# Optimization experiments

Hardware: AMD Instinct MI355X
Metric: run time of the kernel (lower is better)

The kernel has to match this reference:

```python
import jax, jax.numpy as jnp
import numpy as np
from jax import lax

B, T, E, H, L = 32, 512, 1024, 1024, 128


def setup_inputs() -> dict:
    key = jax.random.key(0)
    ks = jax.random.split(key, 25)
    s = 0.02  # small init scale for stable tanh/sigmoid

    def p(k, shape):
        return jax.random.normal(k, shape, jnp.float32) * s

    return {
        "x": jax.random.normal(ks[0], (B, T, E), jnp.float32),
        "eps": jax.random.normal(ks[1], (B, L), jnp.float32),
        # linear1 / linear2 (torch convention: W is [out, in])
        "W1": p(ks[2], (H, E)), "b1": jnp.zeros((H,), jnp.float32),
        "W2": p(ks[3], (H, H)), "b2": jnp.zeros((H,), jnp.float32),
        # encoder GRU (gates ordered r,z,n as in torch)
        "Wih_e": p(ks[4], (3 * H, H)), "Whh_e": p(ks[5], (3 * H, H)),
        "bih_e": jnp.zeros((3 * H,), jnp.float32), "bhh_e": jnp.zeros((3 * H,), jnp.float32),
        # decoder GRU
        "Wih_d": p(ks[6], (3 * H, H)), "Whh_d": p(ks[7], (3 * H, H)),
        "bih_d": jnp.zeros((3 * H,), jnp.float32), "bhh_d": jnp.zeros((3 * H,), jnp.float32),
        # VAE heads
        "Wm": p(ks[8], (L, H)), "bm": jnp.zeros((L,), jnp.float32),
        "Wv": p(ks[9], (L, H)), "bv": jnp.zeros((L,), jnp.float32),
        "Wl": p(ks[10], (H, L)), "bl": jnp.zeros((H,), jnp.float32),
        # output layer (H -> E)
        "Wo": p(ks[11], (E, H)), "bo": jnp.zeros((E,), jnp.float32),
        "lengths": jax.random.randint(ks[12], (B,), 1, T + 1, jnp.int32),
    }


def _gru(xs, h0, Wih, Whh, bih, bhh, lengths):
    """torch-style GRU over padded batch xs:[B,T,H].
    Emulates pack_padded_sequence: h frozen and outputs zeroed for t >= length.
    Returns (outputs [B,T,H], final hidden [B,H])."""
    Tn = xs.shape[1]

    def step(h, inp):
        xt, t = inp  # xt:[B,H]
        gi = xt @ Wih.T + bih          # [B,3H]
        gh = h @ Whh.T + bhh           # [B,3H]
        ir, iz, inn = jnp.split(gi, 3, axis=-1)
        hr, hz, hn = jnp.split(gh, 3, axis=-1)
        r = jax.nn.sigmoid(ir + hr)
        zg = jax.nn.sigmoid(iz + hz)
        n = jnp.tanh(inn + r * hn)
        hnew = (1.0 - zg) * n + zg * h
        valid = (t < lengths)[:, None]
        hout = jnp.where(valid, hnew, h)
        yout = jnp.where(valid, hnew, 0.0)  # pad_packed padding_value=0.0
        return hout, yout

    hT, ys = lax.scan(step, h0, (xs.transpose(1, 0, 2), jnp.arange(Tn)))
    return ys.transpose(1, 0, 2), hT


def reference(x, eps, W1, b1, W2, b2, Wih_e, Whh_e, bih_e, bhh_e,
              Wih_d, Whh_d, bih_d, bhh_d, Wm, bm, Wv, bv, Wl, bl, Wo, bo,
              lengths):
    # pad() sorts the batch by descending length (stable) for packing
    sorted_idx = jnp.argsort(-lengths)
    rev_idx = jnp.argsort(sorted_idx)
    xs = x[sorted_idx]            # sorted padded input
    ls = lengths[sorted_idx]

    # shared input projection linear2(relu(linear1(.)))  (decoder dropout is eval-mode identity)
    proj = jnp.maximum(xs @ W1.T + b1, 0.0) @ W2.T + b2   # [B,T,H]

    h0 = jnp.zeros((xs.shape[0], H), proj.dtype)
    _, h_enc = _gru(proj, h0, Wih_e, Whh_e, bih_e, bhh_e, ls)  # [B,H]

    mean = h_enc @ Wm.T + bm
    logv = h_enc @ Wv.T + bv
    z = eps * jnp.exp(0.5 * logv) + mean                   # [B,L], sorted order
    dec_h0 = z @ Wl.T + bl                                 # [B,H]

    ys, _ = _gru(proj, dec_h0, Wih_d, Whh_d, bih_d, bhh_d, ls)  # [B,T,H]
    outputs_layer = ys[rev_idx] @ Wo.T + bo                # unsorted, [B,T,E]

    return (x, outputs_layer, mean, logv, z)
```

## Files before the change

kernel.cpp:

```cpp
#include <hip/hip_runtime.h>
#include <stdint.h>

#define B_  32
#define T_  512
#define E_  1024
#define H_  1024
#define L_  128
#define BT  (B_*T_)
#define G3  (3*H_)

typedef float f32x4 __attribute__((ext_vector_type(4)));
typedef short bf16x8 __attribute__((ext_vector_type(8)));

__device__ __forceinline__ unsigned short f2bf(float f) {
  unsigned u = __float_as_uint(f);
  u = (u + 0x7fffu + ((u >> 16) & 1u)) >> 16;
  return (unsigned short)u;
}
__device__ __forceinline__ float bf2f(unsigned short s) {
  return __uint_as_float(((unsigned)s) << 16);
}

__global__ void k_f2bf(const float* __restrict__ in, unsigned short* __restrict__ out, int n) {
  int i = (blockIdx.x * blockDim.x + threadIdx.x) * 4;
  if (i >= n) return;
  float4 v = *(const float4*)(in + i);
  unsigned lo = (unsigned)f2bf(v.x) | ((unsigned)f2bf(v.y) << 16);
  unsigned hi = (unsigned)f2bf(v.z) | ((unsigned)f2bf(v.w) << 16);
  *(uint2*)(out + i) = make_uint2(lo, hi);
}

template<int OUT_F32, int RELU>
__global__ __launch_bounds__(256)
void k_gemm(const unsigned short* __restrict__ A, const unsigned short* __restrict__ W,
            const float* __restrict__ bias, void* __restrict__ Cc,
            int M, int N, int K)
{
  __shared__ __align__(16) unsigned short As[128 * 64];
  __shared__ __align__(16) unsigned short Bs[128 * 64];
  const int m0 = blockIdx.x * 128, n0 = blockIdx.y * 128;
  const int tid = threadIdx.x;
  const int lane = tid & 63, wv = tid >> 6;
  const int wr = wv >> 1, wc = wv & 1;
  f32x4 acc[4][4] = {};

  for (int k0 = 0; k0 < K; k0 += 64) {
#pragma unroll
    for (int i = 0; i < 4; ++i) {
      int o = tid * 16 + i * 4096;
      int r = o >> 7;
      int cb = o & 127;
      const unsigned short* ga = A + (size_t)(m0 + r) * K + k0 + (cb >> 1);
      const unsigned short* gb = W + (size_t)(n0 + r) * K + k0 + (cb >> 1);
      __builtin_amdgcn_global_load_lds((const __attribute__((address_space(1))) void*)ga,
          (__attribute__((address_space(3))) void*)((char*)As + o), 16, 0, 0);
      __builtin_amdgcn_global_load_lds((const __attribute__((address_space(1))) void*)gb,
          (__attribute__((address_space(3))) void*)((char*)Bs + o), 16, 0, 0);
    }
    __syncthreads();
#pragma unroll
    for (int kk = 0; kk < 2; ++kk) {
      bf16x8 af[4], bfr[4];
#pragma unroll
      for (int m = 0; m < 4; ++m)
        af[m] = *(const bf16x8*)(As + (wr * 64 + m * 16 + (lane & 15)) * 64 + kk * 32 + (lane >> 4) * 8);
#pragma unroll
      for (int n = 0; n < 4; ++n)
        bfr[n] = *(const bf16x8*)(Bs + (wc * 64 + n * 16 + (lane & 15)) * 64 + kk * 32 + (lane >> 4) * 8);
#pragma unroll
      for (int m = 0; m < 4; ++m)
#pragma unroll
        for (int n = 0; n < 4; ++n)
          acc[m][n] = __builtin_amdgcn_mfma_f32_16x16x32_bf16(af[m], bfr[n], acc[m][n], 0, 0, 0);
    }
    __syncthreads();
  }
#pragma unroll
  for (int m = 0; m < 4; ++m) {
    int row0 = m0 + wr * 64 + m * 16 + (lane >> 4) * 4;
#pragma unroll
    for (int n = 0; n < 4; ++n) {
      int col = n0 + wc * 64 + n * 16 + (lane & 15);
      float bvv = bias[col];
#pragma unroll
      for (int q = 0; q < 4; ++q) {
        float v = acc[m][n][q] + bvv;
        if (RELU) v = fmaxf(v, 0.f);
        size_t idx = (size_t)(row0 + q) * N + col;
        if (OUT_F32) ((float*)Cc)[idx] = v;
        else ((unsigned short*)Cc)[idx] = f2bf(v);
      }
    }
  }
}

__device__ __forceinline__ void gbar(unsigned* bar, unsigned target) {
  __syncthreads();
  if (threadIdx.x == 0) {
    __hip_atomic_fetch_add(bar, 1u, __ATOMIC_ACQ_REL, __HIP_MEMORY_SCOPE_AGENT);
    while (__hip_atomic_load(bar, __ATOMIC_ACQUIRE, __HIP_MEMORY_SCOPE_AGENT) < target) {
      __builtin_amdgcn_s_sleep(8);
    }
  }
  __syncthreads();
}

template<int IS_DEC>
__global__ __launch_bounds__(384, 2)
void k_gru(const unsigned short* __restrict__ gi,
           const unsigned short* __restrict__ Whhb,
           const float* __restrict__ bhh,
           const int* __restrict__ lengths,
           const float* __restrict__ h0,
           float* __restrict__ hT,
           unsigned short* __restrict__ ys,
           unsigned short* __restrict__ hbuf,
           unsigned* __restrict__ bar)
{
  const int wg = blockIdx.x;
  const int U0 = wg * 16;
  const int tid = threadIdx.x;
  const int lane = tid & 63, wv = tid >> 6;
  const int mt = wv & 1, g = wv >> 1;

  __shared__ float gh_lds[32][48];
  __shared__ float h_master[32][16];
  __shared__ float bhh_s[48];
  __shared__ int len_s[32];

  if (tid < 32) len_s[tid] = lengths[tid];
  if (tid < 48) bhh_s[tid] = bhh[(tid >> 4) * 1024 + U0 + (tid & 15)];

  bf16x8 bfrag[32];
  {
    const unsigned short* wrow = Whhb + (size_t)(g * 1024 + U0 + (lane & 15)) * 1024 + ((lane >> 4) * 8);
#pragma unroll
    for (int kc = 0; kc < 32; ++kc)
      bfrag[kc] = *(const bf16x8*)(wrow + kc * 32);
  }

  for (int p = tid; p < 512; p += 384) {
    int b = p >> 4, u = p & 15;
    float h = IS_DEC ? h0[b * 1024 + U0 + u] : 0.f;
    h_master[b][u] = h;
    hbuf[b * 1024 + U0 + u] = f2bf(h);
  }
  unsigned phase = 1;
  gbar(bar, phase * 64); ++phase;

  for (int t = 0; t < T_; ++t) {
    const unsigned short* hb = hbuf + (t & 1) * (32 * 1024);
    f32x4 a0 = {0.f, 0.f, 0.f, 0.f}, a1 = {0.f, 0.f, 0.f, 0.f};
    const unsigned short* arow = hb + (size_t)(mt * 16 + (lane & 15)) * 1024 + ((lane >> 4) * 8);
#pragma unroll
    for (int kc = 0; kc < 32; kc += 2) {
      bf16x8 f0 = *(const bf16x8*)(arow + kc * 32);
      bf16x8 f1 = *(const bf16x8*)(arow + kc * 32 + 32);
      a0 = __builtin_amdgcn_mfma_f32_16x16x32_bf16(f0, bfrag[kc], a0, 0, 0, 0);
      a1 = __builtin_amdgcn_mfma_f32_16x16x32_bf16(f1, bfrag[kc + 1], a1, 0, 0, 0);
    }
#pragma unroll
    for (int q = 0; q < 4; ++q)
      gh_lds[mt * 16 + (lane >> 4) * 4 + q][g * 16 + (lane & 15)] = a0[q] + a1[q];
    __syncthreads();

    if (tid < 256) {
      int b = tid >> 3, u2 = tid & 7;
      int valid = t < len_s[b];
      const unsigned short* gib = gi + (size_t)(b * T_ + t) * G3 + U0 + u2 * 2;
      unsigned vr = *(const unsigned*)(gib);
      unsigned vz = *(const unsigned*)(gib + 1024);
      unsigned vn = *(const unsigned*)(gib + 2048);
      unsigned hw = 0, yw = 0;
#pragma unroll
      for (int j = 0; j < 2; ++j) {
        int u = u2 * 2 + j;
        float ir  = bf2f((unsigned short)(j ? (vr >> 16) : (vr & 0xffff)));
        float iz  = bf2f((unsigned short)(j ? (vz >> 16) : (vz & 0xffff)));
        float in_ = bf2f((unsigned short)(j ? (vn >> 16) : (vn & 0xffff)));
        float gr = gh_lds[b][u]      + bhh_s[u];
        float gz = gh_lds[b][16 + u] + bhh_s[16 + u];
        float gn = gh_lds[b][32 + u] + bhh_s[32 + u];
        float rr = 1.f / (1.f + expf(-(ir + gr)));
        float zz = 1.f / (1.f + expf(-(iz + gz)));
        float nn = tanhf(in_ + rr * gn);
        float hp = h_master[b][u];
        float hn = valid ? ((1.f - zz) * nn + zz * hp) : hp;
        h_master[b][u] = hn;
        unsigned short hb16 = f2bf(hn);
        hw |= ((unsigned)hb16) << (16 * j);
        if (IS_DEC) { unsigned short yb = valid ? hb16 : (unsigned short)0; yw |= ((unsigned)yb) << (16 * j); }
      }
      unsigned* hnext = (unsigned*)(hbuf + ((t + 1) & 1) * (32 * 1024));
      hnext[(b * 1024 + U0 + u2 * 2) >> 1] = hw;
      if (IS_DEC) ((unsigned*)ys)[((size_t)(b * T_ + t) * 1024 + U0 + u2 * 2) >> 1] = yw;
    }
    gbar(bar, phase * 64); ++phase;
  }

  if (!IS_DEC && tid < 256) {
    int b = tid >> 3, u2 = tid & 7;
    hT[b * 1024 + U0 + u2 * 2]     = h_master[b][u2 * 2];
    hT[b * 1024 + U0 + u2 * 2 + 1] = h_master[b][u2 * 2 + 1];
  }
}

__global__ __launch_bounds__(256)
void k_mid(const float* __restrict__ h_enc,
           const float* __restrict__ Wm, const float* __restrict__ bm,
           const float* __restrict__ Wv, const float* __restrict__ bv,
           const float* __restrict__ Wl, const float* __restrict__ bl,
           const float* __restrict__ eps, const int* __restrict__ lengths,
           float* __restrict__ out_mean, float* __restrict__ out_logv,
           float* __restrict__ out_z, float* __restrict__ dec_h0)
{
  const int b = blockIdx.x;
  const int tid = threadIdx.x;
  __shared__ float h_s[1024];
  __shared__ float mean_s[128], logv_s[128], z_s[128];
  __shared__ int pos_s;
  for (int i = tid; i < 1024; i += 256) h_s[i] = h_enc[b * 1024 + i];
  if (tid == 0) {
    int lb = lengths[b], r = 0;
    for (int j = 0; j < 32; ++j) {
      int lj = lengths[j];
      r += (lj > lb) || (lj == lb && j < b);
    }
    pos_s = r;
  }
  __syncthreads();
  {
    const float* wrow = (tid < 128) ? (Wm + tid * 1024) : (Wv + (tid - 128) * 1024);
    float s = 0.f;
    for (int k = 0; k < 1024; ++k) s += h_s[k] * wrow[k];
    s += (tid < 128) ? bm[tid] : bv[tid - 128];
    if (tid < 128) mean_s[tid] = s; else logv_s[tid - 128] = s;
  }
  __syncthreads();
  int pos = pos_s;
  if (tid < 128) {
    float zv = eps[pos * 128 + tid] * expf(0.5f * logv_s[tid]) + mean_s[tid];
    z_s[tid] = zv;
    out_mean[pos * 128 + tid] = mean_s[tid];
    out_logv[pos * 128 + tid] = logv_s[tid];
    out_z[pos * 128 + tid]    = zv;
  }
  __syncthreads();
  for (int h = tid; h < 1024; h += 256) {
    float s = bl[h];
    const float* w = Wl + h * 128;
    for (int k = 0; k < 128; ++k) s += z_s[k] * w[k];
    dec_h0[b * 1024 + h] = s;
  }
}

extern "C" void kernel_launch(void* const* d_in, const int* in_sizes, int n_in,
                              void* d_out, int out_size, void* d_ws, size_t ws_size,
                              hipStream_t stream)
{
  const float* x     = (const float*)d_in[0];
  const float* eps   = (const float*)d_in[1];
  const float* W1    = (const float*)d_in[2];
  const float* b1    = (const float*)d_in[3];
  const float* W2    = (const float*)d_in[4];
  const float* b2    = (const float*)d_in[5];
  const float* Wih_e = (const float*)d_in[6];
  const float* Whh_e = (const float*)d_in[7];
  const float* bih_e = (const float*)d_in[8];
  const float* bhh_e = (const float*)d_in[9];
  const float* Wih_d = (const float*)d_in[10];
  const float* Whh_d = (const float*)d_in[11];
  const float* bih_d = (const float*)d_in[12];
  const float* bhh_d = (const float*)d_in[13];
  const float* Wm    = (const float*)d_in[14];
  const float* bm    = (const float*)d_in[15];
  const float* Wv    = (const float*)d_in[16];
  const float* bv    = (const float*)d_in[17];
  const float* Wl    = (const float*)d_in[18];
  const float* bl    = (const float*)d_in[19];
  const float* Wo    = (const float*)d_in[20];
  const float* bo    = (const float*)d_in[21];
  const int* lengths = (const int*)d_in[22];

  char* ws = (char*)d_ws;
  unsigned short* xb    = (unsigned short*)(ws + 0);
  unsigned short* proj  = (unsigned short*)(ws + 33554432);
  unsigned short* gi    = (unsigned short*)(ws + 67108864);
  unsigned short* W1b   = (unsigned short*)(ws + 167772160);
  unsigned short* W2b   = (unsigned short*)(ws + 169869312);
  unsigned short* Wiheb = (unsigned short*)(ws + 171966464);
  unsigned short* Wihdb = (unsigned short*)(ws + 178257920);
  unsigned short* Whheb = (unsigned short*)(ws + 184549376);
  unsigned short* Whhdb = (unsigned short*)(ws + 190840832);
  unsigned short* Wob   = (unsigned short*)(ws + 197132288);
  unsigned short* hbuf  = (unsigned short*)(ws + 199229440);
  float* h_enc          = (float*)(ws + 199360512);
  float* dec_h0         = (float*)(ws + 199491584);
  unsigned* bars        = (unsigned*)(ws + 199622656);

  float* out_x    = (float*)d_out;
  float* out_ol   = (float*)d_out + 16777216;
  float* out_mean = (float*)d_out + 2 * 16777216;
  float* out_logv = out_mean + 4096;
  float* out_z    = out_logv + 4096;

  hipMemcpyAsync(out_x, x, (size_t)16777216 * 4, hipMemcpyDeviceToDevice, stream);
  hipMemsetAsync(bars, 0, 512, stream);

  auto cv = [&](const float* s, unsigned short* d, int n) {
    k_f2bf<<<dim3((n / 4 + 255) / 256), dim3(256), 0, stream>>>(s, d, n);
  };
  cv(x, xb, BT * E_);
  cv(W1, W1b, H_ * E_);
  cv(W2, W2b, H_ * H_);
  cv(Wih_e, Wiheb, G3 * H_);
  cv(Wih_d, Wihdb, G3 * H_);
  cv(Whh_e, Whheb, G3 * H_);
  cv(Whh_d, Whhdb, G3 * H_);
  cv(Wo, Wob, E_ * H_);

  unsigned short* P1 = gi;
  k_gemm<0, 1><<<dim3(BT / 128, H_ / 128), 256, 0, stream>>>(xb, W1b, b1, P1, BT, H_, E_);
  k_gemm<0, 0><<<dim3(BT / 128, H_ / 128), 256, 0, stream>>>(P1, W2b, b2, proj, BT, H_, H_);
  k_gemm<0, 0><<<dim3(BT / 128, G3 / 128), 256, 0, stream>>>(proj, Wiheb, bih_e, gi, BT, G3, H_);
  k_gru<0><<<64, 384, 0, stream>>>(gi, Whheb, bhh_e, lengths, nullptr, h_enc, nullptr, hbuf, bars);
  k_mid<<<32, 256, 0, stream>>>(h_enc, Wm, bm, Wv, bv, Wl, bl, eps, lengths,
                                out_mean, out_logv, out_z, dec_h0);
  k_gemm<0, 0><<<dim3(BT / 128, G3 / 128), 256, 0, stream>>>(proj, Wihdb, bih_d, gi, BT, G3, H_);
  unsigned short* ys = xb;
  k_gru<1><<<64, 384, 0, stream>>>(gi, Whhdb, bhh_d, lengths, dec_h0, nullptr, ys, hbuf, bars + 64);
  k_gemm<1, 0><<<dim3(BT / 128, E_ / 128), 256, 0, stream>>>(ys, Wob, bo, out_ol, BT, E_, H_);
}
```

Measured before the change: 11.20 ms.

## Replace atomic grid barrier in GRU with per-workgroup flags and prefetch gates

The global atomic-counter barrier is replaced by per-workgroup release flags, padded to 64 bytes each. Each step, wave 0 of every workgroup spins on all 64 flags with one lane per flag, then issues an acquire fence. The input-gate values for the next timestep are loaded one step ahead so their global latency overlaps the recurrent matmul. The gate LDS array is padded to reduce bank conflicts. The cost is heavier flag polling traffic, plus reliance on the double-buffered h for ordering, since workgroups now only wait for everyone to finish the previous step.

```diff
diff --git a/kernel.cpp b/kernel.cpp
--- a/kernel.cpp
+++ b/kernel.cpp
@@ -94,17 +94,6 @@
   }
 }
 
-__device__ __forceinline__ void gbar(unsigned* bar, unsigned target) {
-  __syncthreads();
-  if (threadIdx.x == 0) {
-    __hip_atomic_fetch_add(bar, 1u, __ATOMIC_ACQ_REL, __HIP_MEMORY_SCOPE_AGENT);
-    while (__hip_atomic_load(bar, __ATOMIC_ACQUIRE, __HIP_MEMORY_SCOPE_AGENT) < target) {
-      __builtin_amdgcn_s_sleep(8);
-    }
-  }
-  __syncthreads();
-}
-
 template<int IS_DEC>
 __global__ __launch_bounds__(384, 2)
 void k_gru(const unsigned short* __restrict__ gi,
@@ -115,7 +104,7 @@
            float* __restrict__ hT,
            unsigned short* __restrict__ ys,
            unsigned short* __restrict__ hbuf,
-           unsigned* __restrict__ bar)
+           unsigned* __restrict__ flags)
 {
   const int wg = blockIdx.x;
   const int U0 = wg * 16;
@@ -123,7 +112,7 @@
   const int lane = tid & 63, wv = tid >> 6;
   const int mt = wv & 1, g = wv >> 1;
 
-  __shared__ float gh_lds[32][48];
+  __shared__ float gh_lds[32][49];
   __shared__ float h_master[32][16];
   __shared__ float bhh_s[48];
   __shared__ int len_s[32];
@@ -137,6 +126,15 @@
 #pragma unroll
     for (int kc = 0; kc < 32; ++kc)
       bfrag[kc] = *(const bf16x8*)(wrow + kc * 32);
+  }
+
+  const int gb = tid >> 3, gu2 = tid & 7;
+  const unsigned short* gibase = gi + (size_t)gb * T_ * G3 + U0 + gu2 * 2;
+  unsigned vr_c = 0, vz_c = 0, vn_c = 0, vr_n = 0, vz_n = 0, vn_n = 0;
+  if (tid < 256) {
+    vr_c = *(const unsigned*)(gibase);
+    vz_c = *(const unsigned*)(gibase + 1024);
+    vn_c = *(const unsigned*)(gibase + 2048);
   }
 
   for (int p = tid; p < 512; p += 384) {
@@ -145,10 +143,24 @@
     h_master[b][u] = h;
     hbuf[b * 1024 + U0 + u] = f2bf(h);
   }
-  unsigned phase = 1;
-  gbar(bar, phase * 64); ++phase;
+  __syncthreads();
+  if (tid == 0)
+    __hip_atomic_store(flags + wg * 16, 1u, __ATOMIC_RELEASE, __HIP_MEMORY_SCOPE_AGENT);
 
   for (int t = 0; t < T_; ++t) {
+    if (tid < 256 && t + 1 < T_) {
+      const unsigned short* p = gibase + (size_t)(t + 1) * G3;
+      vr_n = *(const unsigned*)(p);
+      vz_n = *(const unsigned*)(p + 1024);
+      vn_n = *(const unsigned*)(p + 2048);
+    }
+    if (wv == 0) {
+      unsigned* fp = flags + lane * 16;
+      while (__hip_atomic_load(fp, __ATOMIC_RELAXED, __HIP_MEMORY_SCOPE_AGENT) < (unsigned)(t + 1)) {}
+      __builtin_amdgcn_fence(__ATOMIC_ACQUIRE, "agent");
+    }
+    __syncthreads();
+
     const unsigned short* hb = hbuf + (t & 1) * (32 * 1024);
     f32x4 a0 = {0.f, 0.f, 0.f, 0.f}, a1 = {0.f, 0.f, 0.f, 0.f};
     const unsigned short* arow = hb + (size_t)(mt * 16 + (lane & 15)) * 1024 + ((lane >> 4) * 8);
@@ -165,19 +177,15 @@
     __syncthreads();
 
     if (tid < 256) {
-      int b = tid >> 3, u2 = tid & 7;
+      int b = gb, u2 = gu2;
       int valid = t < len_s[b];
-      const unsigned short* gib = gi + (size_t)(b * T_ + t) * G3 + U0 + u2 * 2;
-      unsigned vr = *(const unsigned*)(gib);
-      unsigned vz = *(const unsigned*)(gib + 1024);
-      unsigned vn = *(const unsigned*)(gib + 2048);
       unsigned hw = 0, yw = 0;
 #pragma unroll
       for (int j = 0; j < 2; ++j) {
         int u = u2 * 2 + j;
-        float ir  = bf2f((unsigned short)(j ? (vr >> 16) : (vr & 0xffff)));
-        float iz  = bf2f((unsigned short)(j ? (vz >> 16) : (vz & 0xffff)));
-        float in_ = bf2f((unsigned short)(j ? (vn >> 16) : (vn & 0xffff)));
+        float ir  = bf2f((unsigned short)(j ? (vr_c >> 16) : (vr_c & 0xffff)));
+        float iz  = bf2f((unsigned short)(j ? (vz_c >> 16) : (vz_c & 0xffff)));
+        float in_ = bf2f((unsigned short)(j ? (vn_c >> 16) : (vn_c & 0xffff)));
         float gr = gh_lds[b][u]      + bhh_s[u];
         float gz = gh_lds[b][16 + u] + bhh_s[16 + u];
         float gn = gh_lds[b][32 + u] + bhh_s[32 + u];
@@ -195,7 +203,10 @@
       hnext[(b * 1024 + U0 + u2 * 2) >> 1] = hw;
       if (IS_DEC) ((unsigned*)ys)[((size_t)(b * T_ + t) * 1024 + U0 + u2 * 2) >> 1] = yw;
     }
-    gbar(bar, phase * 64); ++phase;
+    __syncthreads();
+    if (tid == 0)
+      __hip_atomic_store(flags + wg * 16, (unsigned)(t + 2), __ATOMIC_RELEASE, __HIP_MEMORY_SCOPE_AGENT);
+    vr_c = vr_n; vz_c = vz_n; vn_c = vn_n;
   }
 
   if (!IS_DEC && tid < 256) {
@@ -305,7 +316,7 @@
   float* out_z    = out_logv + 4096;
 
   hipMemcpyAsync(out_x, x, (size_t)16777216 * 4, hipMemcpyDeviceToDevice, stream);
-  hipMemsetAsync(bars, 0, 512, stream);
+  hipMemsetAsync(bars, 0, 8192, stream);
 
   auto cv = [&](const float* s, unsigned short* d, int n) {
     k_f2bf<<<dim3((n / 4 + 255) / 256), dim3(256), 0, stream>>>(s, d, n);
@@ -328,6 +339,6 @@
                                 out_mean, out_logv, out_z, dec_h0);
   k_gemm<0, 0><<<dim3(BT / 128, G3 / 128), 256, 0, stream>>>(proj, Wihdb, bih_d, gi, BT, G3, H_);
   unsigned short* ys = xb;
-  k_gru<1><<<64, 384, 0, stream>>>(gi, Whhdb, bhh_d, lengths, dec_h0, nullptr, ys, hbuf, bars + 64);
+  k_gru<1><<<64, 384, 0, stream>>>(gi, Whhdb, bhh_d, lengths, dec_h0, nullptr, ys, hbuf, bars + 1024);
   k_gemm<1, 0><<<dim3(BT / 128, E_ / 128), 256, 0, stream>>>(ys, Wob, bo, out_ol, BT, E_, H_);
 }
```

Measured after the change: 12.69 ms. 1.13x slower.
